# Kernel tuning notes

Measured on AMD Instinct MI355X. Metric: run time of the kernel, lower is better.

Reference implementation:

```python
import jax, jax.numpy as jnp
import numpy as np

K_NEI = 4096
T = 0.07
M_MOM = 0.5
N_DATA = 1281167
D = 128
BATCH = 256
NO_KMEANS = 6
N_CLUSTERS = 1000


def _l2n(x):
    return x / jnp.sqrt(jnp.sum(x ** 2, axis=1, keepdims=True))


def setup_inputs() -> dict:
    key = jax.random.key(0)
    k1, k2, k3, k4 = jax.random.split(key, 4)
    outputs = jax.random.normal(k1, (BATCH, D), dtype=jnp.float32)
    indices = jax.random.randint(k2, (BATCH,), 0, N_DATA, dtype=jnp.int64)
    bank = _l2n(jax.random.normal(k3, (N_DATA, D), dtype=jnp.float32))
    cluster_labels = jax.random.randint(k4, (NO_KMEANS, N_DATA), 0, N_CLUSTERS, dtype=jnp.int64)
    return {"outputs": outputs, "indices": indices, "bank": bank, "cluster_labels": cluster_labels}


def reference(outputs, indices, bank, cluster_labels):
    out = _l2n(outputs)                                  # [B, D]
    all_dps = out @ bank.T                               # [B, N]
    back_nei_dps, back_nei_idxs = jax.lax.top_k(all_dps, K_NEI)  # [B, k]
    Z = 2876934.2 / 1281167 * bank.shape[0]
    back_nei_probs = jnp.exp(back_nei_dps / T) / Z       # [B, k]
    # union over k-means partitions: does neighbor share batch sample's cluster?
    batch_labels = cluster_labels[:, indices]            # [Km, B]
    top_labels = cluster_labels[:, back_nei_idxs]        # [Km, B, k]
    all_close = jnp.any(batch_labels[:, :, None] == top_labels, axis=0)  # [B, k]
    relative_probs = jnp.sum(jnp.where(all_close, back_nei_probs, 0.0), axis=1)
    relative_probs = relative_probs / jnp.sum(back_nei_probs, axis=1)
    loss = -jnp.mean(jnp.log(relative_probs + 1e-7))[None]  # [1]
    # momentum memory update
    data_memory = bank[indices]                          # [B, D]
    new_data_memory = _l2n(data_memory * M_MOM + (1.0 - M_MOM) * out)
    return loss, new_data_memory
```

## Files before the change

### kernel.cpp

```cpp
#include <hip/hip_runtime.h>
#include <hip/hip_bf16.h>

#define NDATA 1281167
#define DIM   128
#define BATCH 256
#define KNEI  4096
#define NKM   6

typedef __attribute__((ext_vector_type(8))) short  short8;
typedef __attribute__((ext_vector_type(4))) float  f32x4;

constexpr float TSCREEN = 0.215f;
constexpr int   MAXCAP  = 12288;
constexpr int   TILE    = 64;
constexpr int   NTILES  = (NDATA + TILE - 1) / TILE;
constexpr int   QCAP    = 1024;
constexpr int   NBINS   = 4096;
constexpr float BIN_LO  = 0.20f;
constexpr float BIN_SCALE = 8000.0f;

#define OUT_N_OFF  0
#define OUT_BF_OFF 131072
#define CNT_OFF    196608
#define DP_OFF     212992

__device__ __forceinline__ unsigned pk2(float x, float y) {
  __hip_bfloat162 h = __float22bfloat162_rn(make_float2(x, y));
  union { __hip_bfloat162 h2; unsigned u; } c; c.h2 = h; return c.u;
}

__global__ void k_prep(const float* __restrict__ outputs,
                       const int* __restrict__ indices, int istride,
                       const float* __restrict__ bank,
                       float* __restrict__ out_n,
                       unsigned short* __restrict__ out_bf,
                       float* __restrict__ d_out)
{
  const int r = blockIdx.x, l = threadIdx.x;
  float2 v = *(const float2*)&outputs[r*DIM + l*2];
  float ss = v.x*v.x + v.y*v.y;
  #pragma unroll
  for (int m = 1; m < 64; m <<= 1) ss += __shfl_xor(ss, m, 64);
  float inv = 1.0f / sqrtf(ss);
  float nx = v.x * inv, ny = v.y * inv;
  out_n[r*DIM + l*2]     = nx;
  out_n[r*DIM + l*2 + 1] = ny;
  unsigned ux = __float_as_uint(nx); ux = (ux + 0x7FFF + ((ux >> 16) & 1)) >> 16;
  unsigned uy = __float_as_uint(ny); uy = (uy + 0x7FFF + ((uy >> 16) & 1)) >> 16;
  out_bf[r*DIM + l*2]     = (unsigned short)ux;
  out_bf[r*DIM + l*2 + 1] = (unsigned short)uy;
  long idx = (long)indices[r*istride];
  float2 mv = *(const float2*)&bank[idx*DIM + l*2];
  float bx = mv.x*0.5f + 0.5f*nx;
  float by = mv.y*0.5f + 0.5f*ny;
  float s2 = bx*bx + by*by;
  #pragma unroll
  for (int m = 1; m < 64; m <<= 1) s2 += __shfl_xor(s2, m, 64);
  float i2 = 1.0f / sqrtf(s2);
  d_out[1 + r*DIM + l*2]     = bx*i2;
  d_out[1 + r*DIM + l*2 + 1] = by*i2;
}

__global__ __launch_bounds__(256, 2)
void k_screen(const float* __restrict__ bank,
              const float* __restrict__ out_n,
              const unsigned short* __restrict__ out_bf,
              float* __restrict__ cand_dp, int* __restrict__ cand_idx,
              int* __restrict__ cand_cnt, int cap)
{
  __shared__ float buf[2][TILE*DIM];
  __shared__ unsigned q[QCAP];
  __shared__ int qn2[2];

  const int tid = threadIdx.x;
  const int w = tid >> 6, l = tid & 63;

  short8 bfrag[4][4];
  {
    const int col0 = w*64 + (l & 15);
    const int kro  = (l >> 4) * 8;
    #pragma unroll
    for (int ot = 0; ot < 4; ot++)
      #pragma unroll
      for (int ks = 0; ks < 4; ks++)
        bfrag[ot][ks] = *(const short8*)&out_bf[(col0 + ot*16)*DIM + ks*32 + kro];
  }

  if (tid == 0) { qn2[0] = 0; qn2[1] = 0; }

  int tile = blockIdx.x;
  int cur = 0;
  if (tile < NTILES) {
    #pragma unroll
    for (int r = 0; r < 8; r++) {
      int Gu = r*256 + tid;
      int row = Gu >> 5, u = Gu & 31;
      long grow = (long)tile*TILE + row;
      float4 vv = *(const float4*)&bank[grow < NDATA ? grow*(long)DIM + u*4 : (long)(u*4)];
      ((float4*)buf[0])[row*32 + (u ^ (row & 15))] = vv;
    }
  }

  for (; tile < NTILES; tile += gridDim.x) {
    __syncthreads();
    if (tid == 0) qn2[cur ^ 1] = 0;

    const int nt = tile + gridDim.x;
    const bool have_next = (nt < NTILES);
    float4 st[8];
    if (have_next) {
      #pragma unroll
      for (int r = 0; r < 8; r++) {
        int Gu = r*256 + tid;
        int row = Gu >> 5, u = Gu & 31;
        long grow = (long)nt*TILE + row;
        st[r] = *(const float4*)&bank[grow < NDATA ? grow*(long)DIM + u*4 : (long)(u*4)];
      }
    }

    const float4* bp4 = (const float4*)buf[cur];
    f32x4 acc[4][4];
    #pragma unroll
    for (int rt = 0; rt < 4; rt++)
      #pragma unroll
      for (int ot = 0; ot < 4; ot++)
        acc[rt][ot] = (f32x4){0.f, 0.f, 0.f, 0.f};

    #pragma unroll
    for (int rt = 0; rt < 4; rt++) {
      const int Ar = rt*16 + (l & 15);
      const int mr = Ar & 15;
      #pragma unroll
      for (int ks = 0; ks < 4; ks++) {
        const int u0 = ks*8 + (l >> 4)*2;
        float4 fa = bp4[Ar*32 + ( u0      ^ mr)];
        float4 fb = bp4[Ar*32 + ((u0 + 1) ^ mr)];
        union { short8 s; unsigned u[4]; } a;
        a.u[0] = pk2(fa.x, fa.y);
        a.u[1] = pk2(fa.z, fa.w);
        a.u[2] = pk2(fb.x, fb.y);
        a.u[3] = pk2(fb.z, fb.w);
        #pragma unroll
        for (int ot = 0; ot < 4; ot++)
          acc[rt][ot] = __builtin_amdgcn_mfma_f32_16x16x32_bf16(a.s, bfrag[ot][ks], acc[rt][ot], 0, 0, 0);
      }
    }

    #pragma unroll
    for (int rt = 0; rt < 4; rt++)
      #pragma unroll
      for (int ot = 0; ot < 4; ot++)
        #pragma unroll
        for (int j = 0; j < 4; j++) {
          float vdp = acc[rt][ot][j];
          if (vdp >= TSCREEN) {
            int brow = rt*16 + (l >> 4)*4 + j;
            if ((long)tile*TILE + brow < NDATA) {
              int pos = atomicAdd(&qn2[cur], 1);
              unsigned col = (unsigned)(w*64 + ot*16 + (l & 15));
              if (pos < QCAP) q[pos] = ((unsigned)brow << 8) | col;
            }
          }
        }

    __syncthreads();

    int H = qn2[cur]; if (H > QCAP) H = QCAP;
    for (int h = tid >> 4; h < H; h += 16) {
      unsigned e = q[h];
      int brow = (int)(e >> 8), col = (int)(e & 255);
      int j = tid & 15;
      float4 o0 = *(const float4*)&out_n[col*DIM + j*8];
      float4 o1 = *(const float4*)&out_n[col*DIM + j*8 + 4];
      int mr = brow & 15;
      float4 b0 = bp4[brow*32 + ((2*j    ) ^ mr)];
      float4 b1 = bp4[brow*32 + ((2*j + 1) ^ mr)];
      float p = o0.x*b0.x + o0.y*b0.y + o0.z*b0.z + o0.w*b0.w
              + o1.x*b1.x + o1.y*b1.y + o1.z*b1.z + o1.w*b1.w;
      #pragma unroll
      for (int s = 1; s < 16; s <<= 1) p += __shfl_xor(p, s, 64);
      if (j == 0) {
        int slot = atomicAdd(&cand_cnt[col*16], 1);
        if (slot < cap) {
          cand_dp [(size_t)col*cap + slot] = p;
          cand_idx[(size_t)col*cap + slot] = tile*TILE + brow;
        }
      }
    }

    if (have_next) {
      #pragma unroll
      for (int r = 0; r < 8; r++) {
        int Gu = r*256 + tid;
        int row = Gu >> 5, u = Gu & 31;
        ((float4*)buf[cur ^ 1])[row*32 + (u ^ (row & 15))] = st[r];
      }
    }
    cur ^= 1;
  }
}

__global__ __launch_bounds__(256)
void k_select(const float* __restrict__ cand_dp, const int* __restrict__ cand_idx,
              const int* __restrict__ cand_cnt, int cap,
              const int* __restrict__ clab, int lstride,
              const int* __restrict__ indices, int istride,
              float* __restrict__ d_out)
{
  __shared__ int hist[NBINS];
  __shared__ int csuf[256];
  __shared__ int sb_bin, sb_above;
  __shared__ unsigned tk_key[256];
  __shared__ int tk_bidx[256];
  __shared__ int tk_n;
  __shared__ double red[512];

  const int row = blockIdx.x, tid = threadIdx.x;
  int n = cand_cnt[row*16]; if (n > cap) n = cap;
  const float* dp = cand_dp + (size_t)row*cap;
  const int*   ci = cand_idx + (size_t)row*cap;

  for (int i = tid; i < NBINS; i += 256) hist[i] = 0;
  if (tid == 0) { tk_n = 0; sb_bin = -1; sb_above = 0; }
  __syncthreads();

  for (int i = tid; i < n; i += 256) {
    float v = dp[i];
    int b = (int)((v - BIN_LO) * BIN_SCALE);
    b = b < 0 ? 0 : (b > NBINS - 1 ? NBINS - 1 : b);
    atomicAdd(&hist[b], 1);
  }
  __syncthreads();

  int tot = 0;
  #pragma unroll
  for (int j = 0; j < 16; j++) tot += hist[tid*16 + j];
  csuf[tid] = tot;
  __syncthreads();
  if (tid == 0) {
    int s = 0;
    for (int c = 255; c >= 0; c--) { int t = csuf[c]; csuf[c] = s; s += t; }
  }
  __syncthreads();
  {
    int s = csuf[tid];
    for (int j = 15; j >= 0; j--) {
      int b = tid*16 + j, h = hist[b];
      if (s < KNEI && s + h >= KNEI) { sb_bin = b; sb_above = s; }
      s += h;
    }
  }
  __syncthreads();
  const int bstar = sb_bin;
  const int need  = (bstar >= 0) ? (KNEI - sb_above) : 0;

  int bl[NKM];
  #pragma unroll
  for (int k = 0; k < NKM; k++)
    bl[k] = clab[((size_t)k*NDATA + (size_t)indices[row*istride]) * lstride];

  double num = 0.0, den = 0.0;

  for (int i = tid; i < n; i += 256) {
    float v = dp[i];
    int b = (int)((v - BIN_LO) * BIN_SCALE);
    b = b < 0 ? 0 : (b > NBINS - 1 ? NBINS - 1 : b);
    if (b > bstar) {
      int idx = ci[i];
      float prob = expf(v / 0.07f);
      bool match = false;
      #pragma unroll
      for (int k = 0; k < NKM; k++)
        match = match || (clab[((size_t)k*NDATA + (size_t)idx) * lstride] == bl[k]);
      den += prob; if (match) num += prob;
    } else if (b == bstar) {
      int p = atomicAdd(&tk_n, 1);
      if (p < 256) { tk_key[p] = __float_as_uint(v); tk_bidx[p] = ci[i]; }
    }
  }
  __syncthreads();

  int m = tk_n; if (m > 256) m = 256;
  if (tid < m) {
    unsigned kj = tk_key[tid]; int bj = tk_bidx[tid];
    int rank = 0;
    for (int qq = 0; qq < m; qq++) {
      unsigned kq = tk_key[qq];
      rank += (int)((kq > kj) || (kq == kj && tk_bidx[qq] < bj));
    }
    if (rank < need) {
      float v = __uint_as_float(kj);
      float prob = expf(v / 0.07f);
      bool match = false;
      #pragma unroll
      for (int k = 0; k < NKM; k++)
        match = match || (clab[((size_t)k*NDATA + (size_t)bj) * lstride] == bl[k]);
      den += prob; if (match) num += prob;
    }
  }

  red[tid] = num; red[tid + 256] = den;
  __syncthreads();
  for (int s = 128; s > 0; s >>= 1) {
    if (tid < s) { red[tid] += red[tid + s]; red[tid + 256] += red[tid + 256 + s]; }
    __syncthreads();
  }
  if (tid == 0) {
    float rp = (float)(red[0] / red[256]);
    atomicAdd(d_out, -logf(rp + 1e-7f) / 256.0f);
  }
}

extern "C" void kernel_launch(void* const* d_in, const int* in_sizes, int n_in,
                              void* d_out, int out_size, void* d_ws, size_t ws_size,
                              hipStream_t stream)
{
  const float* outputs = (const float*)d_in[0];
  const int*   indices = (const int*)d_in[1];
  const float* bank    = (const float*)d_in[2];
  const int*   clab    = (const int*)d_in[3];
  const int istride = (in_sizes[1] == BATCH) ? 1 : 2;
  const int lstride = (in_sizes[3] == NKM*NDATA) ? 1 : 2;
  float* out = (float*)d_out;

  char* ws = (char*)d_ws;
  float*          out_n    = (float*)(ws + OUT_N_OFF);
  unsigned short* out_bf   = (unsigned short*)(ws + OUT_BF_OFF);
  int*            cand_cnt = (int*)(ws + CNT_OFF);

  int cap = MAXCAP;
  size_t avail = ws_size > DP_OFF ? ws_size - DP_OFF : 0;
  long maxcap = (long)(avail / ((size_t)BATCH * 8));
  if (maxcap < cap) cap = (int)(maxcap > 0 ? maxcap : 1);
  float* cand_dp  = (float*)(ws + DP_OFF);
  int*   cand_idx = (int*)(ws + DP_OFF + (size_t)BATCH * cap * 4);

  hipMemsetAsync(out, 0, sizeof(float), stream);
  hipMemsetAsync(cand_cnt, 0, 16384, stream);

  k_prep<<<BATCH, 64, 0, stream>>>(outputs, indices, istride, bank, out_n, out_bf, out);
  k_screen<<<512, 256, 0, stream>>>(bank, out_n, out_bf, cand_dp, cand_idx, cand_cnt, cap);
  k_select<<<BATCH, 256, 0, stream>>>(cand_dp, cand_idx, cand_cnt, cap, clab, lstride,
                                      indices, istride, out);
}
```

Baseline: 1.498 ms.

## Stage bank tiles via direct global-to-LDS loads and fuse cluster match into screening

```diff
diff --git a/kernel.cpp b/kernel.cpp
--- a/kernel.cpp
+++ b/kernel.cpp
@@ -14,7 +14,7 @@
 constexpr int   MAXCAP  = 12288;
 constexpr int   TILE    = 64;
 constexpr int   NTILES  = (NDATA + TILE - 1) / TILE;
-constexpr int   QCAP    = 1024;
+constexpr int   WQCAP   = 192;
 constexpr int   NBINS   = 4096;
 constexpr float BIN_LO  = 0.20f;
 constexpr float BIN_SCALE = 8000.0f;
@@ -22,18 +22,27 @@
 #define OUT_N_OFF  0
 #define OUT_BF_OFF 131072
 #define CNT_OFF    196608
-#define DP_OFF     212992
+#define BLAB_OFF   212992
+#define DP_OFF     221184
 
 __device__ __forceinline__ unsigned pk2(float x, float y) {
   __hip_bfloat162 h = __float22bfloat162_rn(make_float2(x, y));
   union { __hip_bfloat162 h2; unsigned u; } c; c.h2 = h; return c.u;
 }
 
+__device__ __forceinline__ void gload_lds16(const float* g, float* l) {
+  __builtin_amdgcn_global_load_lds(
+      (const __attribute__((address_space(1))) unsigned int*)g,
+      (__attribute__((address_space(3))) unsigned int*)l, 16, 0, 0);
+}
+
 __global__ void k_prep(const float* __restrict__ outputs,
                        const int* __restrict__ indices, int istride,
                        const float* __restrict__ bank,
+                       const int* __restrict__ clab, int lstride,
                        float* __restrict__ out_n,
                        unsigned short* __restrict__ out_bf,
+                       int* __restrict__ blab,
                        float* __restrict__ d_out)
 {
   const int r = blockIdx.x, l = threadIdx.x;
@@ -49,7 +58,10 @@
   unsigned uy = __float_as_uint(ny); uy = (uy + 0x7FFF + ((uy >> 16) & 1)) >> 16;
   out_bf[r*DIM + l*2]     = (unsigned short)ux;
   out_bf[r*DIM + l*2 + 1] = (unsigned short)uy;
+
   long idx = (long)indices[r*istride];
+  if (l < NKM) blab[r*8 + l] = clab[((size_t)l*NDATA + (size_t)idx)*(size_t)lstride];
+
   float2 mv = *(const float2*)&bank[idx*DIM + l*2];
   float bx = mv.x*0.5f + 0.5f*nx;
   float by = mv.y*0.5f + 0.5f*ny;
@@ -61,75 +73,64 @@
   d_out[1 + r*DIM + l*2 + 1] = by*i2;
 }
 
-__global__ __launch_bounds__(256, 2)
+__global__ __launch_bounds__(512, 4)
 void k_screen(const float* __restrict__ bank,
               const float* __restrict__ out_n,
               const unsigned short* __restrict__ out_bf,
+              const int* __restrict__ clab, int lstride,
+              const int* __restrict__ blab,
               float* __restrict__ cand_dp, int* __restrict__ cand_idx,
               int* __restrict__ cand_cnt, int cap)
 {
   __shared__ float buf[2][TILE*DIM];
-  __shared__ unsigned q[QCAP];
-  __shared__ int qn2[2];
+  __shared__ unsigned q[8][WQCAP];
+  __shared__ int qn[8];
 
   const int tid = threadIdx.x;
   const int w = tid >> 6, l = tid & 63;
 
-  short8 bfrag[4][4];
+  short8 bfrag[2][4];
   {
-    const int col0 = w*64 + (l & 15);
+    const int col0 = w*32 + (l & 15);
     const int kro  = (l >> 4) * 8;
     #pragma unroll
-    for (int ot = 0; ot < 4; ot++)
+    for (int ot = 0; ot < 2; ot++)
       #pragma unroll
       for (int ks = 0; ks < 4; ks++)
         bfrag[ot][ks] = *(const short8*)&out_bf[(col0 + ot*16)*DIM + ks*32 + kro];
   }
 
-  if (tid == 0) { qn2[0] = 0; qn2[1] = 0; }
+  auto stage = [&](float* dst, int t) {
+    #pragma unroll
+    for (int r = 0; r < 4; r++) {
+      int p = (w*4 + r)*64 + l;
+      int row = p >> 5, qq = p & 31;
+      long grow = (long)t*TILE + row;
+      const float* g = &bank[(grow < NDATA ? grow*(long)DIM : 0L) + ((qq ^ (row & 15)) << 2)];
+      float* lp = dst + (w*4 + r)*256;
+      gload_lds16(g, lp);
+    }
+  };
 
   int tile = blockIdx.x;
   int cur = 0;
-  if (tile < NTILES) {
-    #pragma unroll
-    for (int r = 0; r < 8; r++) {
-      int Gu = r*256 + tid;
-      int row = Gu >> 5, u = Gu & 31;
-      long grow = (long)tile*TILE + row;
-      float4 vv = *(const float4*)&bank[grow < NDATA ? grow*(long)DIM + u*4 : (long)(u*4)];
-      ((float4*)buf[0])[row*32 + (u ^ (row & 15))] = vv;
-    }
-  }
+  if (tile < NTILES) stage(buf[0], tile);
 
   for (; tile < NTILES; tile += gridDim.x) {
     __syncthreads();
-    if (tid == 0) qn2[cur ^ 1] = 0;
-
     const int nt = tile + gridDim.x;
-    const bool have_next = (nt < NTILES);
-    float4 st[8];
-    if (have_next) {
-      #pragma unroll
-      for (int r = 0; r < 8; r++) {
-        int Gu = r*256 + tid;
-        int row = Gu >> 5, u = Gu & 31;
-        long grow = (long)nt*TILE + row;
-        st[r] = *(const float4*)&bank[grow < NDATA ? grow*(long)DIM + u*4 : (long)(u*4)];
-      }
-    }
+    if (nt < NTILES) stage(buf[cur ^ 1], nt);
+    if (l == 0) qn[w] = 0;
 
     const float4* bp4 = (const float4*)buf[cur];
-    f32x4 acc[4][4];
-    #pragma unroll
-    for (int rt = 0; rt < 4; rt++)
-      #pragma unroll
-      for (int ot = 0; ot < 4; ot++)
-        acc[rt][ot] = (f32x4){0.f, 0.f, 0.f, 0.f};
+    f32x4 acc[4][2];
+    #pragma unroll
+    for (int rt = 0; rt < 4; rt++) { acc[rt][0] = (f32x4){0,0,0,0}; acc[rt][1] = (f32x4){0,0,0,0}; }
 
     #pragma unroll
     for (int rt = 0; rt < 4; rt++) {
       const int Ar = rt*16 + (l & 15);
-      const int mr = Ar & 15;
+      const int mr = l & 15;
       #pragma unroll
       for (int ks = 0; ks < 4; ks++) {
         const int u0 = ks*8 + (l >> 4)*2;
@@ -140,36 +141,34 @@
         a.u[1] = pk2(fa.z, fa.w);
         a.u[2] = pk2(fb.x, fb.y);
         a.u[3] = pk2(fb.z, fb.w);
-        #pragma unroll
-        for (int ot = 0; ot < 4; ot++)
-          acc[rt][ot] = __builtin_amdgcn_mfma_f32_16x16x32_bf16(a.s, bfrag[ot][ks], acc[rt][ot], 0, 0, 0);
+        acc[rt][0] = __builtin_amdgcn_mfma_f32_16x16x32_bf16(a.s, bfrag[0][ks], acc[rt][0], 0, 0, 0);
+        acc[rt][1] = __builtin_amdgcn_mfma_f32_16x16x32_bf16(a.s, bfrag[1][ks], acc[rt][1], 0, 0, 0);
       }
     }
 
     #pragma unroll
     for (int rt = 0; rt < 4; rt++)
       #pragma unroll
-      for (int ot = 0; ot < 4; ot++)
+      for (int ot = 0; ot < 2; ot++)
         #pragma unroll
         for (int j = 0; j < 4; j++) {
           float vdp = acc[rt][ot][j];
           if (vdp >= TSCREEN) {
             int brow = rt*16 + (l >> 4)*4 + j;
             if ((long)tile*TILE + brow < NDATA) {
-              int pos = atomicAdd(&qn2[cur], 1);
-              unsigned col = (unsigned)(w*64 + ot*16 + (l & 15));
-              if (pos < QCAP) q[pos] = ((unsigned)brow << 8) | col;
+              int pos = atomicAdd(&qn[w], 1);
+              if (pos < WQCAP)
+                q[w][pos] = ((unsigned)brow << 8) | (unsigned)(w*32 + ot*16 + (l & 15));
             }
           }
         }
 
-    __syncthreads();
-
-    int H = qn2[cur]; if (H > QCAP) H = QCAP;
-    for (int h = tid >> 4; h < H; h += 16) {
-      unsigned e = q[h];
+    int H = qn[w]; if (H > WQCAP) H = WQCAP;
+    for (int h = (l >> 4); h < H; h += 4) {
+      unsigned e = q[w][h];
       int brow = (int)(e >> 8), col = (int)(e & 255);
-      int j = tid & 15;
+      int idx  = tile*TILE + brow;
+      int j = l & 15;
       float4 o0 = *(const float4*)&out_n[col*DIM + j*8];
       float4 o1 = *(const float4*)&out_n[col*DIM + j*8 + 4];
       int mr = brow & 15;
@@ -179,21 +178,19 @@
               + o1.x*b1.x + o1.y*b1.y + o1.z*b1.z + o1.w*b1.w;
       #pragma unroll
       for (int s = 1; s < 16; s <<= 1) p += __shfl_xor(p, s, 64);
+      int lab = -1, blb = -2;
+      if (j < NKM) {
+        lab = clab[((size_t)j*NDATA + (size_t)idx)*(size_t)lstride];
+        blb = blab[col*8 + j];
+      }
+      unsigned long long bal = __ballot(j < NKM && lab == blb);
+      bool match = ((bal >> (l & 48)) & 0xFFFFull) != 0ull;
       if (j == 0) {
         int slot = atomicAdd(&cand_cnt[col*16], 1);
         if (slot < cap) {
           cand_dp [(size_t)col*cap + slot] = p;
-          cand_idx[(size_t)col*cap + slot] = tile*TILE + brow;
+          cand_idx[(size_t)col*cap + slot] = idx | (match ? (1 << 30) : 0);
         }
-      }
-    }
-
-    if (have_next) {
-      #pragma unroll
-      for (int r = 0; r < 8; r++) {
-        int Gu = r*256 + tid;
-        int row = Gu >> 5, u = Gu & 31;
-        ((float4*)buf[cur ^ 1])[row*32 + (u ^ (row & 15))] = st[r];
       }
     }
     cur ^= 1;
@@ -203,8 +200,6 @@
 __global__ __launch_bounds__(256)
 void k_select(const float* __restrict__ cand_dp, const int* __restrict__ cand_idx,
               const int* __restrict__ cand_cnt, int cap,
-              const int* __restrict__ clab, int lstride,
-              const int* __restrict__ indices, int istride,
               float* __restrict__ d_out)
 {
   __shared__ int hist[NBINS];
@@ -254,11 +249,6 @@
   const int bstar = sb_bin;
   const int need  = (bstar >= 0) ? (KNEI - sb_above) : 0;
 
-  int bl[NKM];
-  #pragma unroll
-  for (int k = 0; k < NKM; k++)
-    bl[k] = clab[((size_t)k*NDATA + (size_t)indices[row*istride]) * lstride];
-
   double num = 0.0, den = 0.0;
 
   for (int i = tid; i < n; i += 256) {
@@ -266,13 +256,9 @@
     int b = (int)((v - BIN_LO) * BIN_SCALE);
     b = b < 0 ? 0 : (b > NBINS - 1 ? NBINS - 1 : b);
     if (b > bstar) {
-      int idx = ci[i];
+      int e = ci[i];
       float prob = expf(v / 0.07f);
-      bool match = false;
-      #pragma unroll
-      for (int k = 0; k < NKM; k++)
-        match = match || (clab[((size_t)k*NDATA + (size_t)idx) * lstride] == bl[k]);
-      den += prob; if (match) num += prob;
+      den += prob; if (e & (1 << 30)) num += prob;
     } else if (b == bstar) {
       int p = atomicAdd(&tk_n, 1);
       if (p < 256) { tk_key[p] = __float_as_uint(v); tk_bidx[p] = ci[i]; }
@@ -282,20 +268,17 @@
 
   int m = tk_n; if (m > 256) m = 256;
   if (tid < m) {
-    unsigned kj = tk_key[tid]; int bj = tk_bidx[tid];
+    unsigned kj = tk_key[tid]; int ej = tk_bidx[tid]; int bj = ej & 0x3FFFFFFF;
     int rank = 0;
     for (int qq = 0; qq < m; qq++) {
       unsigned kq = tk_key[qq];
-      rank += (int)((kq > kj) || (kq == kj && tk_bidx[qq] < bj));
+      int bq = tk_bidx[qq] & 0x3FFFFFFF;
+      rank += (int)((kq > kj) || (kq == kj && bq < bj));
     }
     if (rank < need) {
       float v = __uint_as_float(kj);
       float prob = expf(v / 0.07f);
-      bool match = false;
-      #pragma unroll
-      for (int k = 0; k < NKM; k++)
-        match = match || (clab[((size_t)k*NDATA + (size_t)bj) * lstride] == bl[k]);
-      den += prob; if (match) num += prob;
+      den += prob; if (ej & (1 << 30)) num += prob;
     }
   }
 
@@ -327,6 +310,7 @@
   float*          out_n    = (float*)(ws + OUT_N_OFF);
   unsigned short* out_bf   = (unsigned short*)(ws + OUT_BF_OFF);
   int*            cand_cnt = (int*)(ws + CNT_OFF);
+  int*            blab     = (int*)(ws + BLAB_OFF);
 
   int cap = MAXCAP;
   size_t avail = ws_size > DP_OFF ? ws_size - DP_OFF : 0;
@@ -338,8 +322,9 @@
   hipMemsetAsync(out, 0, sizeof(float), stream);
   hipMemsetAsync(cand_cnt, 0, 16384, stream);
 
-  k_prep<<<BATCH, 64, 0, stream>>>(outputs, indices, istride, bank, out_n, out_bf, out);
-  k_screen<<<512, 256, 0, stream>>>(bank, out_n, out_bf, cand_dp, cand_idx, cand_cnt, cap);
-  k_select<<<BATCH, 256, 0, stream>>>(cand_dp, cand_idx, cand_cnt, cap, clab, lstride,
-                                      indices, istride, out);
-}
+  k_prep<<<BATCH, 64, 0, stream>>>(outputs, indices, istride, bank, clab, lstride,
+                                   out_n, out_bf, blab, out);
+  k_screen<<<512, 512, 0, stream>>>(bank, out_n, out_bf, clab, lstride, blab,
+                                    cand_dp, cand_idx, cand_cnt, cap);
+  k_select<<<BATCH, 256, 0, stream>>>(cand_dp, cand_idx, cand_cnt, cap, out);
+}
```

Result: no change. 1.522 ms (+1.6%).
